# Kernel optimization log

Hardware: AMD Instinct MI355X
Metric: run time of the kernel (lower is better)

The kernel has to match this reference:

```python
import jax, jax.numpy as jnp
import numpy as np

EMBED_DIM = 768
NUM_HEADS = 12
HEAD_DIM = EMBED_DIM // NUM_HEADS  # 64
NUM_LEVELS = 2
Q_INDEX = (0, 6, 12)  # head-axis split per level
K_INDEX = (0, 6, 12)
V_INDEX = (0, 6, 12)


def setup_inputs() -> dict:
    key = jax.random.key(0)
    ks = jax.random.split(key, 12)
    std = 0.02
    d = {
        'inp0': jax.random.normal(ks[0], (8, 2048, 768), jnp.float32),
        'inp1': jax.random.normal(ks[1], (8, 1024, 1536), jnp.float32),
        'attn_mask': jax.random.normal(ks[2], (8, HEAD_DIM), jnp.float32),
        'Wq0': jax.random.normal(ks[3], (768, 768), jnp.float32) * std,
        'bq0': jnp.zeros((768,), jnp.float32),
        'Wk0': jax.random.normal(ks[4], (768, 768), jnp.float32) * std,
        'bk0': jnp.zeros((768,), jnp.float32),
        'Wv0': jax.random.normal(ks[5], (768, 768), jnp.float32) * std,
        'bv0': jnp.zeros((768,), jnp.float32),
        'Wq1': jax.random.normal(ks[6], (1536, 768), jnp.float32) * std,
        'bq1': jnp.zeros((768,), jnp.float32),
        'Wk1': jax.random.normal(ks[7], (1536, 768), jnp.float32) * std,
        'bk1': jnp.zeros((768,), jnp.float32),
        'Wv1': jax.random.normal(ks[8], (1536, 768), jnp.float32) * std,
        'bv1': jnp.zeros((768,), jnp.float32),
        'Wo': jax.random.normal(ks[9], (2 * 768, 768), jnp.float32) * std,
        'bo': jnp.zeros((768,), jnp.float32),
    }
    return d


def _split_heads(x):
    b, n, _ = x.shape
    return x.reshape(b, n, NUM_HEADS, HEAD_DIM).transpose(0, 2, 1, 3)  # b h n d


def _level_attention(level, inp, Wq, bq, Wk, bk, Wv, bv, attn_mask):
    q = _split_heads(inp @ Wq + bq)[:, Q_INDEX[level]:Q_INDEX[level + 1]]
    k = _split_heads(inp @ Wk + bk)[:, K_INDEX[level]:K_INDEX[level + 1]]
    v = _split_heads(inp @ Wv + bv)[:, V_INDEX[level]:V_INDEX[level + 1]]
    q = q * (HEAD_DIM ** -0.5)
    q = q + attn_mask[:, None, None, :]  # broadcast mask over heads & positions
    scores = jnp.einsum('bhnd,bhmd->bhnm', q, k)
    attn = jax.nn.softmax(scores, axis=-1)
    return jnp.einsum('bhnm,bhmd->bhnd', attn, v)  # b h n d


def reference(inp0, inp1, attn_mask, Wq0, bq0, Wk0, bk0, Wv0, bv0,
              Wq1, bq1, Wk1, bk1, Wv1, bv1, Wo, bo):
    levels = [
        (inp0, Wq0, bq0, Wk0, bk0, Wv0, bv0),
        (inp1, Wq1, bq1, Wk1, bk1, Wv1, bv1),
    ]
    outputs = [_level_attention(l, *args, attn_mask) for l, args in enumerate(levels)]
    n_max = max(o.shape[2] for o in outputs)
    merged, masks = [], []
    for o in outputs:
        b, h, n, dd = o.shape
        x = o.transpose(0, 2, 1, 3).reshape(b, n, h * dd)  # b n (h d)
        x = jnp.pad(x, ((0, 0), (0, n_max - n), (0, EMBED_DIM - h * dd)))
        merged.append(x)
        masks.append(jnp.pad(jnp.ones((n,), jnp.float32), (0, n_max - n)))
    x = jnp.concatenate(merged, axis=-1)  # [b, n_max, NUM_LEVELS*EMBED_DIM]
    output_mask = jnp.stack(masks)  # [NUM_LEVELS, n_max]
    output = x @ Wo + bo
    return (output, output_mask)
```

## Files before the change

kernel.cpp:

```cpp
#include <hip/hip_runtime.h>
#include <cmath>

typedef __bf16 bf16x8 __attribute__((ext_vector_type(8)));
typedef float floatx4 __attribute__((ext_vector_type(4)));

__global__ void conv_bf16(const float* __restrict__ in, __bf16* __restrict__ out, int n8)
{
    int t = blockIdx.x * 256 + threadIdx.x;
    if (t < n8) {
        floatx4 f0 = *(const floatx4*)&in[(size_t)t * 8];
        floatx4 f1 = *(const floatx4*)&in[(size_t)t * 8 + 4];
        bf16x8 o;
#pragma unroll
        for (int j = 0; j < 4; j++) { o[j] = (__bf16)f0[j]; o[4 + j] = (__bf16)f1[j]; }
        *(bf16x8*)&out[(size_t)t * 8] = o;
    }
}

__global__ void pack_qkv(const float* __restrict__ Wq, const float* __restrict__ Wk,
                         const float* __restrict__ Wv, __bf16* __restrict__ WT,
                         int Kd, int off)
{
    __shared__ __bf16 tile[64][72];
    int k0 = blockIdx.x * 64, c0 = blockIdx.y * 64;
    int proj = c0 / 384;
    const float* src = (proj == 0) ? Wq : (proj == 1) ? Wk : Wv;
    int lane = threadIdx.x & 63;
    int col = off + (c0 % 384) + lane;
    int tr = threadIdx.x >> 6;
#pragma unroll
    for (int i = 0; i < 16; i++) {
        int r = i * 4 + tr;
        tile[lane][r] = (__bf16)src[(size_t)(k0 + r) * 768 + col];
    }
    __syncthreads();
#pragma unroll
    for (int i = 0; i < 16; i++) {
        int cl = i * 4 + tr;
        WT[(size_t)(c0 + cl) * Kd + k0 + lane] = tile[cl][lane];
    }
}

__global__ void pack_wo(const float* __restrict__ Wo, __bf16* __restrict__ WT)
{
    __shared__ __bf16 tile[64][72];
    int k0 = blockIdx.x * 64, c0 = blockIdx.y * 64;
    int lane = threadIdx.x & 63;
    int col = c0 + lane;
    int tr = threadIdx.x >> 6;
#pragma unroll
    for (int i = 0; i < 16; i++) {
        int k = k0 + i * 4 + tr;
        int srow = k + (k >= 384 ? 384 : 0);
        tile[lane][i * 4 + tr] = (__bf16)Wo[(size_t)srow * 768 + col];
    }
    __syncthreads();
#pragma unroll
    for (int i = 0; i < 16; i++) {
        int cl = i * 4 + tr;
        WT[(size_t)(c0 + cl) * 768 + k0 + lane] = tile[cl][lane];
    }
}

__global__ __launch_bounds__(256, 2) void qkv_gemm(
    const __bf16* __restrict__ A, const __bf16* __restrict__ BT,
    const float* __restrict__ bq, const float* __restrict__ bk,
    const float* __restrict__ bv, const float* __restrict__ mask,
    __bf16* __restrict__ Qo, __bf16* __restrict__ Ko, __bf16* __restrict__ VTo,
    int Kd, int Nl, int nlsh, int off)
{
    __shared__ __bf16 As[128 * 72];
    __shared__ __bf16 Bs[128 * 72];
    const int tid = threadIdx.x;
    const int lane = tid & 63;
    const int wave = tid >> 6;
    const int lr = lane & 15, lg = lane >> 4;
    const int col0 = blockIdx.x * 128, row0 = blockIdx.y * 128;
    const int qr = (wave >> 1) * 64, qc = (wave & 1) * 64;
    const int srow = tid >> 3, scol = (tid & 7) * 8;
    floatx4 acc[4][4] = {};

    for (int k0 = 0; k0 < Kd; k0 += 64) {
#pragma unroll
        for (int i = 0; i < 4; i++) {
            int r = i * 32 + srow;
            *(bf16x8*)&As[r * 72 + scol] =
                *(const bf16x8*)&A[(size_t)(row0 + r) * Kd + k0 + scol];
            *(bf16x8*)&Bs[r * 72 + scol] =
                *(const bf16x8*)&BT[(size_t)(col0 + r) * Kd + k0 + scol];
        }
        __syncthreads();
#pragma unroll
        for (int ch = 0; ch < 2; ch++) {
            bf16x8 af[4], bfr[4];
#pragma unroll
            for (int mt = 0; mt < 4; mt++)
                af[mt] = *(const bf16x8*)&As[(qr + mt * 16 + lr) * 72 + ch * 32 + lg * 8];
#pragma unroll
            for (int nt = 0; nt < 4; nt++)
                bfr[nt] = *(const bf16x8*)&Bs[(qc + nt * 16 + lr) * 72 + ch * 32 + lg * 8];
#pragma unroll
            for (int mt = 0; mt < 4; mt++)
#pragma unroll
                for (int nt = 0; nt < 4; nt++)
                    acc[mt][nt] = __builtin_amdgcn_mfma_f32_16x16x32_bf16(af[mt], bfr[nt], acc[mt][nt], 0, 0, 0);
        }
        __syncthreads();
    }

    const float S_Q = 0.125f * 1.44269504088896f;
    const float S_M = 1.44269504088896f;
#pragma unroll
    for (int nt = 0; nt < 4; nt++) {
        int C = col0 + qc + nt * 16 + lr;
        int proj = C / 384;
        int rem = C - proj * 384;
        int h = rem >> 6, d = C & 63;
        float bias = (proj == 0) ? bq[off + rem]
                   : (proj == 1) ? bk[off + rem]
                                 : bv[off + rem];
#pragma unroll
        for (int mt = 0; mt < 4; mt++) {
#pragma unroll
            for (int r = 0; r < 4; r++) {
                int R = row0 + qr + mt * 16 + lg * 4 + r;
                int b = R >> nlsh;
                int n = R & (Nl - 1);
                size_t hb = (size_t)(b * 6 + h);
                float v = acc[mt][nt][r] + bias;
                if (proj == 0) {
                    v = fmaf(v, S_Q, S_M * mask[(b << 6) + d]);
                    Qo[(hb * Nl + n) * 64 + d] = (__bf16)v;
                } else if (proj == 1) {
                    Ko[(hb * Nl + n) * 64 + d] = (__bf16)v;
                } else {
                    VTo[(hb * 64 + d) * (size_t)Nl + n] = (__bf16)v;
                }
            }
        }
    }
}

__global__ __launch_bounds__(256, 4) void attn_kernel(
    const __bf16* __restrict__ Q, const __bf16* __restrict__ K,
    const __bf16* __restrict__ VT, __bf16* __restrict__ X,
    int Nl, int xoff)
{
    __shared__ __bf16 Ks[64 * 72];
    __shared__ __bf16 Vs[64 * 72];
    __shared__ __bf16 Ps[4][16 * 72];
    const int tid = threadIdx.x;
    const int wave = tid >> 6, lane = tid & 63;
    const int lr = lane & 15, lg = lane >> 4;
    const int h = blockIdx.y, b = blockIdx.z;
    const size_t head = (size_t)(b * 6 + h) * Nl * 64;
    const int q0 = blockIdx.x * 64 + wave * 16;

    bf16x8 qf[2];
#pragma unroll
    for (int ch = 0; ch < 2; ch++)
        qf[ch] = *(const bf16x8*)&Q[head + (size_t)(q0 + lr) * 64 + ch * 32 + lg * 8];

    bf16x8 onesv;
#pragma unroll
    for (int j = 0; j < 8; j++) onesv[j] = (__bf16)1.0f;

    const int rr = tid >> 2, cc = (tid & 3) * 16;
    const __bf16* Kg = K + head;
    const __bf16* Vg = VT + head;

    bf16x8 kr0, kr1, vr0, vr1;
    {
        size_t kb = (size_t)rr * 64 + cc;
        kr0 = *(const bf16x8*)&Kg[kb];
        kr1 = *(const bf16x8*)&Kg[kb + 8];
        size_t vb = (size_t)rr * Nl + cc;
        vr0 = *(const bf16x8*)&Vg[vb];
        vr1 = *(const bf16x8*)&Vg[vb + 8];
    }

    floatx4 o_acc[4] = {};
    floatx4 l_acc = {};

    for (int n0 = 0; n0 < Nl; n0 += 64) {
        __syncthreads();
        *(bf16x8*)&Ks[rr * 72 + cc]     = kr0;
        *(bf16x8*)&Ks[rr * 72 + cc + 8] = kr1;
        *(bf16x8*)&Vs[rr * 72 + cc]     = vr0;
        *(bf16x8*)&Vs[rr * 72 + cc + 8] = vr1;
        __syncthreads();

        if (n0 + 64 < Nl) {
            size_t kb = (size_t)(n0 + 64 + rr) * 64 + cc;
            kr0 = *(const bf16x8*)&Kg[kb];
            kr1 = *(const bf16x8*)&Kg[kb + 8];
            size_t vb = (size_t)rr * Nl + n0 + 64 + cc;
            vr0 = *(const bf16x8*)&Vg[vb];
            vr1 = *(const bf16x8*)&Vg[vb + 8];
        }

        floatx4 sv[4] = {};
#pragma unroll
        for (int ch = 0; ch < 2; ch++) {
#pragma unroll
            for (int nt = 0; nt < 4; nt++) {
                bf16x8 kb8 = *(const bf16x8*)&Ks[(nt * 16 + lr) * 72 + ch * 32 + lg * 8];
                sv[nt] = __builtin_amdgcn_mfma_f32_16x16x32_bf16(qf[ch], kb8, sv[nt], 0, 0, 0);
            }
        }

#pragma unroll
        for (int nt = 0; nt < 4; nt++) {
#pragma unroll
            for (int r = 0; r < 4; r++) {
                float p = __builtin_amdgcn_exp2f(sv[nt][r]);
                Ps[wave][(lg * 4 + r) * 72 + nt * 16 + lr] = (__bf16)p;
            }
        }
        asm volatile("s_waitcnt lgkmcnt(0)" ::: "memory");

#pragma unroll
        for (int ch = 0; ch < 2; ch++) {
            bf16x8 pa = *(const bf16x8*)&Ps[wave][lr * 72 + ch * 32 + lg * 8];
#pragma unroll
            for (int dt = 0; dt < 4; dt++) {
                bf16x8 vb8 = *(const bf16x8*)&Vs[(dt * 16 + lr) * 72 + ch * 32 + lg * 8];
                o_acc[dt] = __builtin_amdgcn_mfma_f32_16x16x32_bf16(pa, vb8, o_acc[dt], 0, 0, 0);
            }
            l_acc = __builtin_amdgcn_mfma_f32_16x16x32_bf16(pa, onesv, l_acc, 0, 0, 0);
        }
    }

#pragma unroll
    for (int dt = 0; dt < 4; dt++) {
#pragma unroll
        for (int r = 0; r < 4; r++) {
            int n = q0 + lg * 4 + r;
            float o = o_acc[dt][r] / l_acc[r];
            X[(size_t)(b * 2048 + n) * 768 + xoff + h * 64 + dt * 16 + lr] = (__bf16)o;
        }
    }
}

__global__ void fill_pad(__bf16* __restrict__ X, float* __restrict__ om)
{
    int t = blockIdx.x * 256 + threadIdx.x;
    if (t < 393216) {
        int r = t / 48;
        int c = (t - r * 48) * 8;
        int b = r >> 10, n = 1024 + (r & 1023);
        floatx4 z = {0.f, 0.f, 0.f, 0.f};
        *(floatx4*)&X[(size_t)(b * 2048 + n) * 768 + 384 + c] = z;
    }
    if (t < 4096) {
        om[t] = (t < 2048) ? 1.0f : (((t - 2048) < 1024) ? 1.0f : 0.0f);
    }
}

__global__ __launch_bounds__(256, 2) void out_gemm(
    const __bf16* __restrict__ A, const __bf16* __restrict__ BT,
    const float* __restrict__ bo, float* __restrict__ out)
{
    __shared__ __bf16 As[128 * 72];
    __shared__ __bf16 Bs[128 * 72];
    const int tid = threadIdx.x;
    const int lane = tid & 63;
    const int wave = tid >> 6;
    const int lr = lane & 15, lg = lane >> 4;
    const int col0 = blockIdx.x * 128, row0 = blockIdx.y * 128;
    const int qr = (wave >> 1) * 64, qc = (wave & 1) * 64;
    const int srow = tid >> 3, scol = (tid & 7) * 8;
    const int Kd = 768;
    floatx4 acc[4][4] = {};

    for (int k0 = 0; k0 < Kd; k0 += 64) {
#pragma unroll
        for (int i = 0; i < 4; i++) {
            int r = i * 32 + srow;
            *(bf16x8*)&As[r * 72 + scol] =
                *(const bf16x8*)&A[(size_t)(row0 + r) * Kd + k0 + scol];
            *(bf16x8*)&Bs[r * 72 + scol] =
                *(const bf16x8*)&BT[(size_t)(col0 + r) * Kd + k0 + scol];
        }
        __syncthreads();
#pragma unroll
        for (int ch = 0; ch < 2; ch++) {
            bf16x8 af[4], bfr[4];
#pragma unroll
            for (int mt = 0; mt < 4; mt++)
                af[mt] = *(const bf16x8*)&As[(qr + mt * 16 + lr) * 72 + ch * 32 + lg * 8];
#pragma unroll
            for (int nt = 0; nt < 4; nt++)
                bfr[nt] = *(const bf16x8*)&Bs[(qc + nt * 16 + lr) * 72 + ch * 32 + lg * 8];
#pragma unroll
            for (int mt = 0; mt < 4; mt++)
#pragma unroll
                for (int nt = 0; nt < 4; nt++)
                    acc[mt][nt] = __builtin_amdgcn_mfma_f32_16x16x32_bf16(af[mt], bfr[nt], acc[mt][nt], 0, 0, 0);
        }
        __syncthreads();
    }

#pragma unroll
    for (int nt = 0; nt < 4; nt++) {
        int C = col0 + qc + nt * 16 + lr;
        float bias = bo[C];
#pragma unroll
        for (int mt = 0; mt < 4; mt++) {
#pragma unroll
            for (int r = 0; r < 4; r++) {
                int R = row0 + qr + mt * 16 + lg * 4 + r;
                out[(size_t)R * 768 + C] = acc[mt][nt][r] + bias;
            }
        }
    }
}

extern "C" void kernel_launch(void* const* d_in, const int* in_sizes, int n_in,
                              void* d_out, int out_size, void* d_ws, size_t ws_size,
                              hipStream_t stream)
{
    const float* inp0  = (const float*)d_in[0];
    const float* inp1  = (const float*)d_in[1];
    const float* amask = (const float*)d_in[2];
    const float* Wq0 = (const float*)d_in[3];
    const float* bq0 = (const float*)d_in[4];
    const float* Wk0 = (const float*)d_in[5];
    const float* bk0 = (const float*)d_in[6];
    const float* Wv0 = (const float*)d_in[7];
    const float* bv0 = (const float*)d_in[8];
    const float* Wq1 = (const float*)d_in[9];
    const float* bq1 = (const float*)d_in[10];
    const float* Wk1 = (const float*)d_in[11];
    const float* bk1 = (const float*)d_in[12];
    const float* Wv1 = (const float*)d_in[13];
    const float* bv1 = (const float*)d_in[14];
    const float* Wo  = (const float*)d_in[15];
    const float* bo  = (const float*)d_in[16];

    char* ws = (char*)d_ws;
    __bf16* WT  = (__bf16*)(ws + 0);
    __bf16* WoT = (__bf16*)(ws + 3538944);
    __bf16* Ab  = (__bf16*)(ws + 4718592);
    __bf16* Qp  = (__bf16*)(ws + 29884416);
    __bf16* Kp  = (__bf16*)(ws + 42467328);
    __bf16* VT  = (__bf16*)(ws + 55050240);
    __bf16* X   = (__bf16*)(ws + 67633152);
    float* outp = (float*)d_out;

    hipLaunchKernelGGL(pack_wo, dim3(12, 12), dim3(256), 0, stream, Wo, WoT);

    hipLaunchKernelGGL(pack_qkv, dim3(12, 18), dim3(256), 0, stream, Wq0, Wk0, Wv0, WT, 768, 0);
    hipLaunchKernelGGL(conv_bf16, dim3(6144), dim3(256), 0, stream, inp0, Ab, 1572864);
    hipLaunchKernelGGL(qkv_gemm, dim3(9, 128), dim3(256), 0, stream,
                       Ab, WT, bq0, bk0, bv0, amask, Qp, Kp, VT, 768, 2048, 11, 0);
    hipLaunchKernelGGL(attn_kernel, dim3(32, 6, 8), dim3(256), 0, stream,
                       Qp, Kp, VT, X, 2048, 0);

    hipLaunchKernelGGL(pack_qkv, dim3(24, 18), dim3(256), 0, stream, Wq1, Wk1, Wv1, WT, 1536, 384);
    hipLaunchKernelGGL(conv_bf16, dim3(6144), dim3(256), 0, stream, inp1, Ab, 1572864);
    hipLaunchKernelGGL(qkv_gemm, dim3(9, 64), dim3(256), 0, stream,
                       Ab, WT, bq1, bk1, bv1, amask, Qp, Kp, VT, 1536, 1024, 10, 384);
    hipLaunchKernelGGL(attn_kernel, dim3(16, 6, 8), dim3(256), 0, stream,
                       Qp, Kp, VT, X, 1024, 384);

    hipLaunchKernelGGL(fill_pad, dim3(1536), dim3(256), 0, stream, X, outp + 12582912);
    hipLaunchKernelGGL(out_gemm, dim3(6, 128), dim3(256), 0, stream, X, WoT, bo, outp);
}
```

Measured before the change: 480.3 us.

## Use direct global-to-LDS loads in GEMMs and double query rows per attention wave

```diff
diff --git a/kernel.cpp b/kernel.cpp
--- a/kernel.cpp
+++ b/kernel.cpp
@@ -3,6 +3,13 @@
 
 typedef __bf16 bf16x8 __attribute__((ext_vector_type(8)));
 typedef float floatx4 __attribute__((ext_vector_type(4)));
+
+typedef __attribute__((address_space(1))) const void* as1_cvp;
+typedef __attribute__((address_space(3))) void* as3_vp;
+
+__device__ __forceinline__ void stage16(const void* g, void* l) {
+    __builtin_amdgcn_global_load_lds((as1_cvp)g, (as3_vp)l, 16, 0, 0);
+}
 
 __global__ void conv_bf16(const float* __restrict__ in, __bf16* __restrict__ out, int n8)
 {
@@ -69,25 +76,23 @@
     __bf16* __restrict__ Qo, __bf16* __restrict__ Ko, __bf16* __restrict__ VTo,
     int Kd, int Nl, int nlsh, int off)
 {
-    __shared__ __bf16 As[128 * 72];
-    __shared__ __bf16 Bs[128 * 72];
+    __shared__ __bf16 As[128 * 64];
+    __shared__ __bf16 Bs[128 * 64];
     const int tid = threadIdx.x;
     const int lane = tid & 63;
     const int wave = tid >> 6;
     const int lr = lane & 15, lg = lane >> 4;
     const int col0 = blockIdx.x * 128, row0 = blockIdx.y * 128;
     const int qr = (wave >> 1) * 64, qc = (wave & 1) * 64;
-    const int srow = tid >> 3, scol = (tid & 7) * 8;
     floatx4 acc[4][4] = {};
 
     for (int k0 = 0; k0 < Kd; k0 += 64) {
+        const __bf16* ga = A + (size_t)(row0 + wave * 32 + (lane >> 3)) * Kd + k0 + (lane & 7) * 8;
+        const __bf16* gb = BT + (size_t)(col0 + wave * 32 + (lane >> 3)) * Kd + k0 + (lane & 7) * 8;
 #pragma unroll
         for (int i = 0; i < 4; i++) {
-            int r = i * 32 + srow;
-            *(bf16x8*)&As[r * 72 + scol] =
-                *(const bf16x8*)&A[(size_t)(row0 + r) * Kd + k0 + scol];
-            *(bf16x8*)&Bs[r * 72 + scol] =
-                *(const bf16x8*)&BT[(size_t)(col0 + r) * Kd + k0 + scol];
+            stage16(ga + (size_t)i * 8 * Kd, &As[(wave * 32 + i * 8) * 64]);
+            stage16(gb + (size_t)i * 8 * Kd, &Bs[(wave * 32 + i * 8) * 64]);
         }
         __syncthreads();
 #pragma unroll
@@ -95,10 +100,10 @@
             bf16x8 af[4], bfr[4];
 #pragma unroll
             for (int mt = 0; mt < 4; mt++)
-                af[mt] = *(const bf16x8*)&As[(qr + mt * 16 + lr) * 72 + ch * 32 + lg * 8];
+                af[mt] = *(const bf16x8*)&As[(qr + mt * 16 + lr) * 64 + ch * 32 + lg * 8];
 #pragma unroll
             for (int nt = 0; nt < 4; nt++)
-                bfr[nt] = *(const bf16x8*)&Bs[(qc + nt * 16 + lr) * 72 + ch * 32 + lg * 8];
+                bfr[nt] = *(const bf16x8*)&Bs[(qc + nt * 16 + lr) * 64 + ch * 32 + lg * 8];
 #pragma unroll
             for (int mt = 0; mt < 4; mt++)
 #pragma unroll
@@ -148,18 +153,20 @@
 {
     __shared__ __bf16 Ks[64 * 72];
     __shared__ __bf16 Vs[64 * 72];
-    __shared__ __bf16 Ps[4][16 * 72];
+    __shared__ __bf16 Ps[4][32 * 72];
     const int tid = threadIdx.x;
     const int wave = tid >> 6, lane = tid & 63;
     const int lr = lane & 15, lg = lane >> 4;
     const int h = blockIdx.y, b = blockIdx.z;
     const size_t head = (size_t)(b * 6 + h) * Nl * 64;
-    const int q0 = blockIdx.x * 64 + wave * 16;
-
-    bf16x8 qf[2];
-#pragma unroll
-    for (int ch = 0; ch < 2; ch++)
-        qf[ch] = *(const bf16x8*)&Q[head + (size_t)(q0 + lr) * 64 + ch * 32 + lg * 8];
+    const int q0 = blockIdx.x * 128 + wave * 16;
+
+    bf16x8 qf[2][2];
+#pragma unroll
+    for (int s = 0; s < 2; s++)
+#pragma unroll
+        for (int ch = 0; ch < 2; ch++)
+            qf[s][ch] = *(const bf16x8*)&Q[head + (size_t)(q0 + s * 64 + lr) * 64 + ch * 32 + lg * 8];
 
     bf16x8 onesv;
 #pragma unroll
@@ -179,8 +186,8 @@
         vr1 = *(const bf16x8*)&Vg[vb + 8];
     }
 
-    floatx4 o_acc[4] = {};
-    floatx4 l_acc = {};
+    floatx4 o_acc[2][4] = {};
+    floatx4 l_acc[2] = {};
 
     for (int n0 = 0; n0 < Nl; n0 += 64) {
         __syncthreads();
@@ -199,47 +206,53 @@
             vr1 = *(const bf16x8*)&Vg[vb + 8];
         }
 
-        floatx4 sv[4] = {};
+        floatx4 sv[2][4] = {};
 #pragma unroll
         for (int ch = 0; ch < 2; ch++) {
 #pragma unroll
             for (int nt = 0; nt < 4; nt++) {
                 bf16x8 kb8 = *(const bf16x8*)&Ks[(nt * 16 + lr) * 72 + ch * 32 + lg * 8];
-                sv[nt] = __builtin_amdgcn_mfma_f32_16x16x32_bf16(qf[ch], kb8, sv[nt], 0, 0, 0);
-            }
-        }
-
-#pragma unroll
-        for (int nt = 0; nt < 4; nt++) {
-#pragma unroll
-            for (int r = 0; r < 4; r++) {
-                float p = __builtin_amdgcn_exp2f(sv[nt][r]);
-                Ps[wave][(lg * 4 + r) * 72 + nt * 16 + lr] = (__bf16)p;
-            }
-        }
+                sv[0][nt] = __builtin_amdgcn_mfma_f32_16x16x32_bf16(qf[0][ch], kb8, sv[0][nt], 0, 0, 0);
+                sv[1][nt] = __builtin_amdgcn_mfma_f32_16x16x32_bf16(qf[1][ch], kb8, sv[1][nt], 0, 0, 0);
+            }
+        }
+
+#pragma unroll
+        for (int s = 0; s < 2; s++)
+#pragma unroll
+            for (int nt = 0; nt < 4; nt++)
+#pragma unroll
+                for (int r = 0; r < 4; r++) {
+                    float p = __builtin_amdgcn_exp2f(sv[s][nt][r]);
+                    Ps[wave][(s * 16 + lg * 4 + r) * 72 + nt * 16 + lr] = (__bf16)p;
+                }
         asm volatile("s_waitcnt lgkmcnt(0)" ::: "memory");
 
 #pragma unroll
         for (int ch = 0; ch < 2; ch++) {
-            bf16x8 pa = *(const bf16x8*)&Ps[wave][lr * 72 + ch * 32 + lg * 8];
+            bf16x8 pa0 = *(const bf16x8*)&Ps[wave][lr * 72 + ch * 32 + lg * 8];
+            bf16x8 pa1 = *(const bf16x8*)&Ps[wave][(16 + lr) * 72 + ch * 32 + lg * 8];
 #pragma unroll
             for (int dt = 0; dt < 4; dt++) {
                 bf16x8 vb8 = *(const bf16x8*)&Vs[(dt * 16 + lr) * 72 + ch * 32 + lg * 8];
-                o_acc[dt] = __builtin_amdgcn_mfma_f32_16x16x32_bf16(pa, vb8, o_acc[dt], 0, 0, 0);
-            }
-            l_acc = __builtin_amdgcn_mfma_f32_16x16x32_bf16(pa, onesv, l_acc, 0, 0, 0);
-        }
-    }
-
-#pragma unroll
-    for (int dt = 0; dt < 4; dt++) {
-#pragma unroll
-        for (int r = 0; r < 4; r++) {
-            int n = q0 + lg * 4 + r;
-            float o = o_acc[dt][r] / l_acc[r];
-            X[(size_t)(b * 2048 + n) * 768 + xoff + h * 64 + dt * 16 + lr] = (__bf16)o;
-        }
-    }
+                o_acc[0][dt] = __builtin_amdgcn_mfma_f32_16x16x32_bf16(pa0, vb8, o_acc[0][dt], 0, 0, 0);
+                o_acc[1][dt] = __builtin_amdgcn_mfma_f32_16x16x32_bf16(pa1, vb8, o_acc[1][dt], 0, 0, 0);
+            }
+            l_acc[0] = __builtin_amdgcn_mfma_f32_16x16x32_bf16(pa0, onesv, l_acc[0], 0, 0, 0);
+            l_acc[1] = __builtin_amdgcn_mfma_f32_16x16x32_bf16(pa1, onesv, l_acc[1], 0, 0, 0);
+        }
+    }
+
+#pragma unroll
+    for (int s = 0; s < 2; s++)
+#pragma unroll
+        for (int dt = 0; dt < 4; dt++)
+#pragma unroll
+            for (int r = 0; r < 4; r++) {
+                int n = q0 + s * 64 + lg * 4 + r;
+                float o = o_acc[s][dt][r] / l_acc[s][r];
+                X[(size_t)(b * 2048 + n) * 768 + xoff + h * 64 + dt * 16 + lr] = (__bf16)o;
+            }
 }
 
 __global__ void fill_pad(__bf16* __restrict__ X, float* __restrict__ om)
@@ -261,26 +274,24 @@
     const __bf16* __restrict__ A, const __bf16* __restrict__ BT,
     const float* __restrict__ bo, float* __restrict__ out)
 {
-    __shared__ __bf16 As[128 * 72];
-    __shared__ __bf16 Bs[128 * 72];
+    __shared__ __bf16 As[128 * 64];
+    __shared__ __bf16 Bs[128 * 64];
     const int tid = threadIdx.x;
     const int lane = tid & 63;
     const int wave = tid >> 6;
     const int lr = lane & 15, lg = lane >> 4;
     const int col0 = blockIdx.x * 128, row0 = blockIdx.y * 128;
     const int qr = (wave >> 1) * 64, qc = (wave & 1) * 64;
-    const int srow = tid >> 3, scol = (tid & 7) * 8;
     const int Kd = 768;
     floatx4 acc[4][4] = {};
 
     for (int k0 = 0; k0 < Kd; k0 += 64) {
+        const __bf16* ga = A + (size_t)(row0 + wave * 32 + (lane >> 3)) * Kd + k0 + (lane & 7) * 8;
+        const __bf16* gb = BT + (size_t)(col0 + wave * 32 + (lane >> 3)) * Kd + k0 + (lane & 7) * 8;
 #pragma unroll
         for (int i = 0; i < 4; i++) {
-            int r = i * 32 + srow;
-            *(bf16x8*)&As[r * 72 + scol] =
-                *(const bf16x8*)&A[(size_t)(row0 + r) * Kd + k0 + scol];
-            *(bf16x8*)&Bs[r * 72 + scol] =
-                *(const bf16x8*)&BT[(size_t)(col0 + r) * Kd + k0 + scol];
+            stage16(ga + (size_t)i * 8 * Kd, &As[(wave * 32 + i * 8) * 64]);
+            stage16(gb + (size_t)i * 8 * Kd, &Bs[(wave * 32 + i * 8) * 64]);
         }
         __syncthreads();
 #pragma unroll
@@ -288,10 +299,10 @@
             bf16x8 af[4], bfr[4];
 #pragma unroll
             for (int mt = 0; mt < 4; mt++)
-                af[mt] = *(const bf16x8*)&As[(qr + mt * 16 + lr) * 72 + ch * 32 + lg * 8];
+                af[mt] = *(const bf16x8*)&As[(qr + mt * 16 + lr) * 64 + ch * 32 + lg * 8];
 #pragma unroll
             for (int nt = 0; nt < 4; nt++)
-                bfr[nt] = *(const bf16x8*)&Bs[(qc + nt * 16 + lr) * 72 + ch * 32 + lg * 8];
+                bfr[nt] = *(const bf16x8*)&Bs[(qc + nt * 16 + lr) * 64 + ch * 32 + lg * 8];
 #pragma unroll
             for (int mt = 0; mt < 4; mt++)
 #pragma unroll
@@ -354,14 +365,14 @@
     hipLaunchKernelGGL(conv_bf16, dim3(6144), dim3(256), 0, stream, inp0, Ab, 1572864);
     hipLaunchKernelGGL(qkv_gemm, dim3(9, 128), dim3(256), 0, stream,
                        Ab, WT, bq0, bk0, bv0, amask, Qp, Kp, VT, 768, 2048, 11, 0);
-    hipLaunchKernelGGL(attn_kernel, dim3(32, 6, 8), dim3(256), 0, stream,
+    hipLaunchKernelGGL(attn_kernel, dim3(16, 6, 8), dim3(256), 0, stream,
                        Qp, Kp, VT, X, 2048, 0);
 
     hipLaunchKernelGGL(pack_qkv, dim3(24, 18), dim3(256), 0, stream, Wq1, Wk1, Wv1, WT, 1536, 384);
     hipLaunchKernelGGL(conv_bf16, dim3(6144), dim3(256), 0, stream, inp1, Ab, 1572864);
     hipLaunchKernelGGL(qkv_gemm, dim3(9, 64), dim3(256), 0, stream,
                        Ab, WT, bq1, bk1, bv1, amask, Qp, Kp, VT, 1536, 1024, 10, 384);
-    hipLaunchKernelGGL(attn_kernel, dim3(16, 6, 8), dim3(256), 0, stream,
+    hipLaunchKernelGGL(attn_kernel, dim3(8, 6, 8), dim3(256), 0, stream,
                        Qp, Kp, VT, X, 1024, 384);
 
     hipLaunchKernelGGL(fill_pad, dim3(1536), dim3(256), 0, stream, X, outp + 12582912);
```

New measurement: 466.2 us. -2.9%, faster.
